# Kernel optimization log

Measured on AMD Instinct MI355X. Metric: run time of the kernel, lower is better.

The kernel has to match this reference:

```python
import jax, jax.numpy as jnp
import numpy as np

N_HEAD = 16
HIDDEN = 1024

def setup_inputs() -> dict:
    key = jax.random.key(0)
    ks = jax.random.split(key, 4)
    B, T, D = 2, 2048, HIDDEN
    x = jax.random.normal(ks[0], (B, T, D), dtype=jnp.float32)
    attention_mask = jnp.zeros((B, 1, 1, T), dtype=jnp.float32)  # additive mask
    w_attn = jax.random.normal(ks[1], (D, 3 * D), dtype=jnp.float32) * (1.0 / np.sqrt(D))
    b_attn = jnp.zeros((3 * D,), dtype=jnp.float32)
    w_proj = jax.random.normal(ks[2], (D, D), dtype=jnp.float32) * (1.0 / np.sqrt(D))
    b_proj = jnp.zeros((D,), dtype=jnp.float32)
    return {"x": x, "attention_mask": attention_mask,
            "w_attn": w_attn, "b_attn": b_attn,
            "w_proj": w_proj, "b_proj": b_proj}

def reference(x, attention_mask, w_attn, b_attn, w_proj, b_proj):
    B, T, D = x.shape
    H = N_HEAD
    hd = D // H
    qkv = x @ w_attn + b_attn                      # [B,T,3D]
    q, k, v = jnp.split(qkv, 3, axis=-1)
    q = q.reshape(B, T, H, hd)
    k = k.reshape(B, T, H, hd)
    v = v.reshape(B, T, H, hd)
    qk = jnp.einsum('BFNH,BTNH->BNFT', q, k) / jnp.sqrt(jnp.asarray(hd, qk_dtype := q.dtype))
    # NOTE: source adds the mask twice (once unconditionally, once inside the None-check)
    attn_weights = qk + attention_mask + attention_mask
    attn_probs = jax.nn.softmax(attn_weights, axis=-1)  # dropout(0.01) is identity at inference
    attn_out = jnp.einsum('BNFT,BTNH->BFNH', attn_probs, v)
    attn_out = attn_out.reshape(B, T, D)
    return attn_out @ w_proj + b_proj
```

## Files before the change

### kernel.cpp

```cpp
#include <hip/hip_runtime.h>
#include <hip/hip_bf16.h>

#define T_SEQ 2048
#define D_MODEL 1024
#define N_HEADS 16

typedef _Float16 half8 __attribute__((ext_vector_type(8)));
typedef _Float16 half4 __attribute__((ext_vector_type(4)));
typedef _Float16 half2v __attribute__((ext_vector_type(2)));
typedef float floatx4 __attribute__((ext_vector_type(4)));
typedef unsigned short ushort4v __attribute__((ext_vector_type(4)));

#define LOG2E 1.44269504088896f

__device__ __forceinline__ unsigned short f32_to_bf16(float f) {
  unsigned u = __builtin_bit_cast(unsigned, f);
  u = u + 0x7FFFu + ((u >> 16) & 1u);
  return (unsigned short)(u >> 16);
}
__device__ __forceinline__ float bf16_to_f32(unsigned short h) {
  unsigned u = ((unsigned)h) << 16;
  return __builtin_bit_cast(float, u);
}
__device__ __forceinline__ half2v pk_f16(float a, float b) {
  return __builtin_bit_cast(half2v, __builtin_amdgcn_cvt_pkrtz(a, b));
}

__device__ __forceinline__ void load16_lds(const _Float16* g, _Float16* lds_base, int lane) {
#if __has_builtin(__builtin_amdgcn_global_load_lds)
  __builtin_amdgcn_global_load_lds(
      (const __attribute__((address_space(1))) void*)g,
      (__attribute__((address_space(3))) void*)lds_base, 16, 0, 0);
#else
  *(half8*)(lds_base + lane * 8) = *(const half8*)g;
#endif
}

__global__ void k_detect(const unsigned short* __restrict__ x, int* __restrict__ flag) {
  __shared__ int cnt;
  if (threadIdx.x == 0) cnt = 0;
  __syncthreads();
  unsigned short v = x[(size_t)threadIdx.x * 2];
  int e = (v >> 7) & 0xFF;
  int ok = (v == 0) || (e >= 100 && e <= 150);
  atomicAdd(&cnt, ok);
  __syncthreads();
  if (threadIdx.x == 0) *flag = (cnt >= 192) ? 1 : 0;
}

__global__ void k_cvt_h(const void* __restrict__ in, _Float16* __restrict__ out,
                        int n, const int* __restrict__ flag) {
  int f = *flag;
  int i = blockIdx.x * 256 + threadIdx.x;
  if (i >= n) return;
  float v = f ? bf16_to_f32(((const unsigned short*)in)[i]) : ((const float*)in)[i];
  out[i] = (_Float16)v;
}

__global__ void k_cvt3(const void* __restrict__ ba, const void* __restrict__ bp,
                       const void* __restrict__ mk, float* __restrict__ baF,
                       float* __restrict__ bpF, float* __restrict__ mask2,
                       const int* __restrict__ flag) {
  int f = *flag;
  int i = blockIdx.x * 256 + threadIdx.x;
  auto cv = [&](const void* p, int j) {
    return f ? bf16_to_f32(((const unsigned short*)p)[j]) : ((const float*)p)[j];
  };
  if (i < 3072) baF[i] = cv(ba, i);
  else if (i < 4096) bpF[i - 3072] = cv(bp, i - 3072);
  else mask2[i - 4096] = cv(mk, i - 4096) * (2.0f * LOG2E);
}

__global__ __launch_bounds__(256) void k_transpose2(
    const void* __restrict__ inA, _Float16* __restrict__ outA,
    const void* __restrict__ inB, _Float16* __restrict__ outB,
    const int* __restrict__ flag) {
  __shared__ float tile[32][33];
  int f = *flag;
  const void* in;
  _Float16* out;
  int N, bid;
  if (blockIdx.x < 3072) { in = inA; out = outA; N = 3072; bid = blockIdx.x; }
  else { in = inB; out = outB; N = 1024; bid = blockIdx.x - 3072; }
  const int K = 1024;
  int nb = N >> 5;
  int bx = bid % nb, by = bid / nb;
  int n0 = bx << 5, k0 = by << 5;
  int c = threadIdx.x & 31, r = threadIdx.x >> 5;
  const float* fin = (const float*)in;
  const unsigned short* uin = (const unsigned short*)in;
#pragma unroll
  for (int i = 0; i < 4; ++i) {
    int kk = r + i * 8;
    size_t idx = (size_t)(k0 + kk) * N + n0 + c;
    tile[kk][c] = f ? bf16_to_f32(uin[idx]) : fin[idx];
  }
  __syncthreads();
#pragma unroll
  for (int i = 0; i < 4; ++i) {
    int nn = r + i * 8;
    out[(size_t)(n0 + nn) * K + k0 + c] = (_Float16)tile[c][nn];
  }
}

template <int TM>
__global__ __launch_bounds__(256) void k_gemm(
    const _Float16* __restrict__ A, const _Float16* __restrict__ BT,
    const float* __restrict__ bias, void* __restrict__ D0,
    void* __restrict__ D1, void* __restrict__ D2,
    int M, int N, int K, int outKind, const int* __restrict__ flag) {
  constexpr int IM = TM / 32;
  __shared__ _Float16 As[TM * 32] __attribute__((aligned(16)));
  __shared__ _Float16 Bs[128 * 32] __attribute__((aligned(16)));
  const int tid = threadIdx.x;
  const int wave = tid >> 6, lane = tid & 63;
  const int ln = lane & 15, quad = lane >> 4;
  const int bm = blockIdx.y * TM, bn = blockIdx.x * 128;
  const int wm = (wave & 1) * (TM / 2), wn = (wave >> 1) * 64;

  const int r0 = tid >> 2, k0 = (tid & 3) * 8;
  const int r1 = (tid + 256) >> 2, k1 = (tid & 3) * 8;
  _Float16* As0 = As + (size_t)(wave * 64) * 8;
  _Float16* As1 = As + (size_t)(wave * 64 + 256) * 8;
  _Float16* Bs0 = Bs + (size_t)(wave * 64) * 8;
  _Float16* Bs1 = Bs + (size_t)(wave * 64 + 256) * 8;
  const _Float16* Ag0 = A + (size_t)(bm + r0) * K + k0;
  const _Float16* Ag1 = A + (size_t)(bm + r1) * K + k1;
  const _Float16* Bg0 = BT + (size_t)(bn + r0) * K + k0;
  const _Float16* Bg1 = BT + (size_t)(bn + r1) * K + k1;

  floatx4 acc[IM][4] = {};

  for (int kt = 0; kt < K; kt += 32) {
    __syncthreads();
    load16_lds(Ag0 + kt, As0, lane);
    if constexpr (TM == 128) load16_lds(Ag1 + kt, As1, lane);
    load16_lds(Bg0 + kt, Bs0, lane);
    load16_lds(Bg1 + kt, Bs1, lane);
    __syncthreads();
    half8 af[IM], bf[4];
#pragma unroll
    for (int i = 0; i < IM; ++i)
      af[i] = *(const half8*)(As + (wm + i * 16 + ln) * 32 + quad * 8);
#pragma unroll
    for (int j = 0; j < 4; ++j)
      bf[j] = *(const half8*)(Bs + (wn + j * 16 + ln) * 32 + quad * 8);
#pragma unroll
    for (int i = 0; i < IM; ++i)
#pragma unroll
      for (int j = 0; j < 4; ++j)
        acc[i][j] = __builtin_amdgcn_mfma_f32_16x16x32_f16(af[i], bf[j], acc[i][j], 0, 0, 0);
  }

  if (outKind == 0) {
    _Float16* Qs = (_Float16*)D0;
    _Float16* Ks = (_Float16*)D1;
    _Float16* Vt = (_Float16*)D2;
    const float qsc = 0.125f * LOG2E;
#pragma unroll
    for (int i = 0; i < IM; ++i) {
      int rbase = bm + wm + i * 16 + quad * 4;
      int sect = rbase >> 10;
      int cfeat = rbase & 1023;
      int h = cfeat >> 6, hd = cfeat & 63;
      float bv[4];
#pragma unroll
      for (int r = 0; r < 4; ++r) bv[r] = bias[rbase + r];
#pragma unroll
      for (int j = 0; j < 4; ++j) {
        int col = bn + wn + j * 16 + ln;
        int b = col >> 11, t = col & 2047;
        size_t bh = (size_t)b * N_HEADS + h;
        float v[4];
#pragma unroll
        for (int r = 0; r < 4; ++r) v[r] = acc[i][j][r] + bv[r];
        if (sect == 0) {
          half4 q;
#pragma unroll
          for (int r = 0; r < 4; ++r) q[r] = (_Float16)(v[r] * qsc);
          *(half4*)(Qs + (bh * T_SEQ + t) * 64 + hd) = q;
        } else if (sect == 1) {
          half4 kk4;
#pragma unroll
          for (int r = 0; r < 4; ++r) kk4[r] = (_Float16)v[r];
          *(half4*)(Ks + (bh * T_SEQ + t) * 64 + hd) = kk4;
        } else {
#pragma unroll
          for (int r = 0; r < 4; ++r)
            Vt[(bh * 64 + hd + r) * T_SEQ + t] = (_Float16)v[r];
        }
      }
    }
  } else {
    int mode = (*flag) ? 2 : 1;
#pragma unroll
    for (int i = 0; i < IM; ++i) {
      int rbase = bm + wm + i * 16 + quad * 4;
      float bv[4];
#pragma unroll
      for (int r = 0; r < 4; ++r) bv[r] = bias[rbase + r];
#pragma unroll
      for (int j = 0; j < 4; ++j) {
        int col = bn + wn + j * 16 + ln;
        float v[4];
#pragma unroll
        for (int r = 0; r < 4; ++r) v[r] = acc[i][j][r] + bv[r];
        if (mode == 1) {
          floatx4 o = {v[0], v[1], v[2], v[3]};
          *(floatx4*)((float*)D0 + (size_t)col * M + rbase) = o;
        } else {
          ushort4v o;
#pragma unroll
          for (int r = 0; r < 4; ++r) o[r] = f32_to_bf16(v[r]);
          *(ushort4v*)((unsigned short*)D0 + (size_t)col * M + rbase) = o;
        }
      }
    }
  }
}

__global__ __launch_bounds__(256) void k_flash(
    const _Float16* __restrict__ Qs, const _Float16* __restrict__ Ks,
    const _Float16* __restrict__ Vt, const float* __restrict__ mask2,
    _Float16* __restrict__ O) {
  __shared__ _Float16 Kl[2][64 * 64] __attribute__((aligned(16)));
  __shared__ _Float16 Vl[2][64 * 64] __attribute__((aligned(16)));
  __shared__ _Float16 Pl[4][16 * 64] __attribute__((aligned(16)));
  const int tid = threadIdx.x, wave = tid >> 6, lane = tid & 63;
  const int ln = lane & 15, quad = lane >> 4;
  const int id = blockIdx.x;
  const int qc = id & 31, h = (id >> 5) & 15, b = id >> 9;
  const size_t bh = (size_t)b * N_HEADS + h;
  const _Float16* Qb = Qs + bh * T_SEQ * 64;
  const _Float16* Kb = Ks + bh * T_SEQ * 64;
  const _Float16* Vb = Vt + bh * 64 * T_SEQ;
  const int q0 = qc * 64 + wave * 16;

  half8 qf[2];
#pragma unroll
  for (int kk = 0; kk < 2; ++kk)
    qf[kk] = *(const half8*)(Qb + (size_t)(q0 + ln) * 64 + kk * 32 + quad * 8);

  floatx4 Oacc[4] = {};
  float m0 = 0.f, l_i = 0.f;
  const float* mrow = mask2 + (size_t)b * T_SEQ;

  const int sr = tid >> 3, scn = (tid & 7) ^ (sr & 7);
  auto stage = [&](int t0, int p) {
    _Float16* K0 = &Kl[p][0] + (size_t)wave * 512;
    _Float16* V0 = &Vl[p][0] + (size_t)wave * 512;
    load16_lds(Kb + (size_t)(t0 + sr) * 64 + scn * 8, K0, lane);
    load16_lds(Kb + (size_t)(t0 + sr + 32) * 64 + scn * 8, K0 + 2048, lane);
    load16_lds(Vb + (size_t)sr * T_SEQ + t0 + scn * 8, V0, lane);
    load16_lds(Vb + (size_t)(sr + 32) * T_SEQ + t0 + scn * 8, V0 + 2048, lane);
  };

  const int ksw0 = ((quad) ^ (ln & 7)) * 8;
  const int ksw1 = ((4 + quad) ^ (ln & 7)) * 8;
  _Float16* Pw = &Pl[wave][0];
  const int lnx = ln & 7;

  stage(0, 0);

  for (int t0 = 0; t0 < T_SEQ; t0 += 64) {
    const int cur = (t0 >> 6) & 1;
    __syncthreads();
    if (t0 + 64 < T_SEQ) stage(t0 + 64, cur ^ 1);
    const _Float16* Kc = &Kl[cur][0];
    const _Float16* Vc = &Vl[cur][0];

    floatx4 s[4];
#pragma unroll
    for (int j = 0; j < 4; ++j) {
      floatx4 z = {0.f, 0.f, 0.f, 0.f};
      half8 kf0 = *(const half8*)(Kc + (j * 16 + ln) * 64 + ksw0);
      z = __builtin_amdgcn_mfma_f32_16x16x32_f16(kf0, qf[0], z, 0, 0, 0);
      half8 kf1 = *(const half8*)(Kc + (j * 16 + ln) * 64 + ksw1);
      z = __builtin_amdgcn_mfma_f32_16x16x32_f16(kf1, qf[1], z, 0, 0, 0);
      floatx4 mv = *(const floatx4*)(mrow + t0 + j * 16 + quad * 4);
      z += mv;
      s[j] = z;
    }

    if (t0 == 0) {
      float tmax = -__builtin_inff();
#pragma unroll
      for (int j = 0; j < 4; ++j)
#pragma unroll
        for (int r = 0; r < 4; ++r) tmax = fmaxf(tmax, s[j][r]);
      tmax = fmaxf(tmax, __shfl_xor(tmax, 16, 64));
      tmax = fmaxf(tmax, __shfl_xor(tmax, 32, 64));
      m0 = fmaxf(tmax, -50.f);
    }

#pragma unroll
    for (int j = 0; j < 4; ++j)
#pragma unroll
      for (int r = 0; r < 4; ++r) {
        float p = __builtin_amdgcn_exp2f(s[j][r] - m0);
        s[j][r] = p;
        l_i += p;
      }

#pragma unroll
    for (int j = 0; j < 4; ++j) {
      half2v p01 = pk_f16(s[j][0], s[j][1]);
      half2v p23 = pk_f16(s[j][2], s[j][3]);
      half4 pk = {p01[0], p01[1], p23[0], p23[1]};
      int c = j * 2 + (quad >> 1);
      *(half4*)(Pw + ln * 64 + (c ^ lnx) * 8 + (quad & 1) * 4) = pk;
    }
    asm volatile("s_waitcnt lgkmcnt(0)" ::: "memory");
#pragma unroll
    for (int kk = 0; kk < 2; ++kk) {
      half8 pf = *(const half8*)(Pw + ln * 64 + ((kk * 4 + quad) ^ lnx) * 8);
      int ks = kk ? ksw1 : ksw0;
#pragma unroll
      for (int jd = 0; jd < 4; ++jd) {
        half8 vf = *(const half8*)(Vc + (jd * 16 + ln) * 64 + ks);
        Oacc[jd] = __builtin_amdgcn_mfma_f32_16x16x32_f16(vf, pf, Oacc[jd], 0, 0, 0);
      }
    }
  }

  l_i += __shfl_xor(l_i, 16, 64);
  l_i += __shfl_xor(l_i, 32, 64);
  float inv = 1.f / l_i;
#pragma unroll
  for (int jd = 0; jd < 4; ++jd) {
    half4 ov;
#pragma unroll
    for (int r = 0; r < 4; ++r) ov[r] = (_Float16)(Oacc[jd][r] * inv);
    *(half4*)(O + ((size_t)b * T_SEQ + q0 + ln) * D_MODEL + h * 64 + jd * 16 + quad * 4) = ov;
  }
}

extern "C" void kernel_launch(void* const* d_in, const int* in_sizes, int n_in,
                              void* d_out, int out_size, void* d_ws, size_t ws_size,
                              hipStream_t stream) {
  const void* x      = d_in[0];
  const void* amask  = d_in[1];
  const void* w_attn = d_in[2];
  const void* b_attn = d_in[3];
  const void* w_proj = d_in[4];
  const void* b_proj = d_in[5];

  char* ws = (char*)d_ws;
  size_t off = 0;
  auto alloc = [&](size_t bytes) {
    void* p = ws + off;
    off += (bytes + 255) & ~(size_t)255;
    return p;
  };
  int* flag        = (int*)alloc(256);
  _Float16* Xh     = (_Float16*)alloc((size_t)4096 * 1024 * 2);
  _Float16* WaT    = (_Float16*)alloc((size_t)3072 * 1024 * 2);
  _Float16* WpT    = (_Float16*)alloc((size_t)1024 * 1024 * 2);
  float* baF       = (float*)alloc(3072 * 4);
  float* bpF       = (float*)alloc(1024 * 4);
  float* mask2     = (float*)alloc(4096 * 4);
  _Float16* Qs     = (_Float16*)alloc((size_t)4096 * 1024 * 2);
  _Float16* Ks     = (_Float16*)alloc((size_t)4096 * 1024 * 2);
  _Float16* Vt     = (_Float16*)alloc((size_t)4096 * 1024 * 2);
  _Float16* AttnH  = (_Float16*)alloc((size_t)4096 * 1024 * 2);

  k_detect<<<1, 256, 0, stream>>>((const unsigned short*)x, flag);
  k_cvt_h<<<(4096 * 1024) / 256, 256, 0, stream>>>(x, Xh, 4096 * 1024, flag);
  k_transpose2<<<3072 + 1024, 256, 0, stream>>>(w_attn, WaT, w_proj, WpT, flag);
  k_cvt3<<<32, 256, 0, stream>>>(b_attn, b_proj, amask, baF, bpF, mask2, flag);

  dim3 g1(4096 / 128, 3072 / 128);
  k_gemm<128><<<g1, 256, 0, stream>>>(WaT, Xh, baF, Qs, Ks, Vt, 3072, 4096, 1024, 0, flag);

  k_flash<<<1024, 256, 0, stream>>>(Qs, Ks, Vt, mask2, AttnH);

  dim3 g2(4096 / 128, 1024 / 64);
  k_gemm<64><<<g2, 256, 0, stream>>>(WpT, AttnH, bpF, d_out, nullptr, nullptr, 1024, 4096, 1024, 1, flag);
}
```

Measured before the change: 223.3 us.

## Vectorize input conversion, streamline flash loop, widen output projection tile

The fp16 input conversion now handles eight elements per thread using vector loads and stores instead of one. In the flash kernel the staging lambda is replaced by incrementing pointers, and the additive mask is loaded as the MFMA accumulator's initial value so the separate add disappears. The explicit lgkmcnt wait before reading P from LDS becomes a plain compiler barrier. The output projection GEMM switches to a 128-wide tile, halving its grid size; dropping the wait risks reading P before the LDS writes complete unless the compiler inserts its own wait.

```diff
diff --git a/kernel.cpp b/kernel.cpp
--- a/kernel.cpp
+++ b/kernel.cpp
@@ -10,6 +10,7 @@
 typedef _Float16 half2v __attribute__((ext_vector_type(2)));
 typedef float floatx4 __attribute__((ext_vector_type(4)));
 typedef unsigned short ushort4v __attribute__((ext_vector_type(4)));
+typedef unsigned short ushort8v __attribute__((ext_vector_type(8)));
 
 #define LOG2E 1.44269504088896f
 
@@ -48,13 +49,23 @@
   if (threadIdx.x == 0) *flag = (cnt >= 192) ? 1 : 0;
 }
 
-__global__ void k_cvt_h(const void* __restrict__ in, _Float16* __restrict__ out,
-                        int n, const int* __restrict__ flag) {
+__global__ void k_cvt_h8(const void* __restrict__ in, _Float16* __restrict__ out,
+                         int n8, const int* __restrict__ flag) {
   int f = *flag;
   int i = blockIdx.x * 256 + threadIdx.x;
-  if (i >= n) return;
-  float v = f ? bf16_to_f32(((const unsigned short*)in)[i]) : ((const float*)in)[i];
-  out[i] = (_Float16)v;
+  if (i >= n8) return;
+  half8 o;
+  if (f) {
+    ushort8v u = ((const ushort8v*)in)[i];
+#pragma unroll
+    for (int e = 0; e < 8; ++e) o[e] = (_Float16)bf16_to_f32(u[e]);
+  } else {
+    floatx4 a = ((const floatx4*)in)[2 * i];
+    floatx4 b = ((const floatx4*)in)[2 * i + 1];
+#pragma unroll
+    for (int e = 0; e < 4; ++e) { o[e] = (_Float16)a[e]; o[e + 4] = (_Float16)b[e]; }
+  }
+  ((half8*)out)[i] = o;
 }
 
 __global__ void k_cvt3(const void* __restrict__ ba, const void* __restrict__ bp,
@@ -243,46 +254,57 @@
 
   floatx4 Oacc[4] = {};
   float m0 = 0.f, l_i = 0.f;
-  const float* mrow = mask2 + (size_t)b * T_SEQ;
 
   const int sr = tid >> 3, scn = (tid & 7) ^ (sr & 7);
-  auto stage = [&](int t0, int p) {
-    _Float16* K0 = &Kl[p][0] + (size_t)wave * 512;
-    _Float16* V0 = &Vl[p][0] + (size_t)wave * 512;
-    load16_lds(Kb + (size_t)(t0 + sr) * 64 + scn * 8, K0, lane);
-    load16_lds(Kb + (size_t)(t0 + sr + 32) * 64 + scn * 8, K0 + 2048, lane);
-    load16_lds(Vb + (size_t)sr * T_SEQ + t0 + scn * 8, V0, lane);
-    load16_lds(Vb + (size_t)(sr + 32) * T_SEQ + t0 + scn * 8, V0 + 2048, lane);
-  };
+  const _Float16* kp0 = Kb + (size_t)sr * 64 + scn * 8;
+  const _Float16* kp1 = kp0 + 32 * 64;
+  const _Float16* vp0 = Vb + (size_t)sr * T_SEQ + scn * 8;
+  const _Float16* vp1 = vp0 + 32 * T_SEQ;
+  const float* mq = mask2 + (size_t)b * T_SEQ + quad * 4;
 
   const int ksw0 = ((quad) ^ (ln & 7)) * 8;
   const int ksw1 = ((4 + quad) ^ (ln & 7)) * 8;
   _Float16* Pw = &Pl[wave][0];
   const int lnx = ln & 7;
 
-  stage(0, 0);
-
-  for (int t0 = 0; t0 < T_SEQ; t0 += 64) {
-    const int cur = (t0 >> 6) & 1;
+  {
+    _Float16* K0 = &Kl[0][0] + (size_t)wave * 512;
+    _Float16* V0 = &Vl[0][0] + (size_t)wave * 512;
+    load16_lds(kp0, K0, lane);
+    load16_lds(kp1, K0 + 2048, lane);
+    load16_lds(vp0, V0, lane);
+    load16_lds(vp1, V0 + 2048, lane);
+    kp0 += 64 * 64; kp1 += 64 * 64; vp0 += 64; vp1 += 64;
+  }
+
+  for (int t = 0; t < 32; ++t) {
+    const int cur = t & 1;
     __syncthreads();
-    if (t0 + 64 < T_SEQ) stage(t0 + 64, cur ^ 1);
+    if (t + 1 < 32) {
+      _Float16* K0 = &Kl[cur ^ 1][0] + (size_t)wave * 512;
+      _Float16* V0 = &Vl[cur ^ 1][0] + (size_t)wave * 512;
+      load16_lds(kp0, K0, lane);
+      load16_lds(kp1, K0 + 2048, lane);
+      load16_lds(vp0, V0, lane);
+      load16_lds(vp1, V0 + 2048, lane);
+      kp0 += 64 * 64; kp1 += 64 * 64; vp0 += 64; vp1 += 64;
+    }
     const _Float16* Kc = &Kl[cur][0];
     const _Float16* Vc = &Vl[cur][0];
 
     floatx4 s[4];
 #pragma unroll
     for (int j = 0; j < 4; ++j) {
-      floatx4 z = {0.f, 0.f, 0.f, 0.f};
+      floatx4 z = *(const floatx4*)(mq + j * 16);
       half8 kf0 = *(const half8*)(Kc + (j * 16 + ln) * 64 + ksw0);
       z = __builtin_amdgcn_mfma_f32_16x16x32_f16(kf0, qf[0], z, 0, 0, 0);
       half8 kf1 = *(const half8*)(Kc + (j * 16 + ln) * 64 + ksw1);
       z = __builtin_amdgcn_mfma_f32_16x16x32_f16(kf1, qf[1], z, 0, 0, 0);
-      floatx4 mv = *(const floatx4*)(mrow + t0 + j * 16 + quad * 4);
-      z += mv;
       s[j] = z;
     }
-
-    if (t0 == 0) {
+    mq += 64;
+
+    if (t == 0) {
       float tmax = -__builtin_inff();
 #pragma unroll
       for (int j = 0; j < 4; ++j)
@@ -310,7 +332,7 @@
       int c = j * 2 + (quad >> 1);
       *(half4*)(Pw + ln * 64 + (c ^ lnx) * 8 + (quad & 1) * 4) = pk;
     }
-    asm volatile("s_waitcnt lgkmcnt(0)" ::: "memory");
+    asm volatile("" ::: "memory");
 #pragma unroll
     for (int kk = 0; kk < 2; ++kk) {
       half8 pf = *(const half8*)(Pw + ln * 64 + ((kk * 4 + quad) ^ lnx) * 8);
@@ -365,7 +387,7 @@
   _Float16* AttnH  = (_Float16*)alloc((size_t)4096 * 1024 * 2);
 
   k_detect<<<1, 256, 0, stream>>>((const unsigned short*)x, flag);
-  k_cvt_h<<<(4096 * 1024) / 256, 256, 0, stream>>>(x, Xh, 4096 * 1024, flag);
+  k_cvt_h8<<<(4096 * 1024 / 8) / 256, 256, 0, stream>>>(x, Xh, 4096 * 1024 / 8, flag);
   k_transpose2<<<3072 + 1024, 256, 0, stream>>>(w_attn, WaT, w_proj, WpT, flag);
   k_cvt3<<<32, 256, 0, stream>>>(b_attn, b_proj, amask, baF, bpF, mask2, flag);
 
@@ -374,6 +396,6 @@
 
   k_flash<<<1024, 256, 0, stream>>>(Qs, Ks, Vt, mask2, AttnH);
 
-  dim3 g2(4096 / 128, 1024 / 64);
-  k_gemm<64><<<g2, 256, 0, stream>>>(WpT, AttnH, bpF, d_out, nullptr, nullptr, 1024, 4096, 1024, 1, flag);
-}
+  dim3 g2(4096 / 128, 1024 / 128);
+  k_gemm<128><<<g2, 256, 0, stream>>>(WpT, AttnH, bpF, d_out, nullptr, nullptr, 1024, 4096, 1024, 1, flag);
+}
```

New measurement: 223.1 us. No clear change (-0.1%).
